# Performance work log

Measured on AMD Instinct MI355X. Metric: run time of the kernel, lower is better.

The kernel has to match this reference:

```python
import jax, jax.numpy as jnp
import numpy as np

K, N = 1024, 16384


def setup_inputs() -> dict:
    key = jax.random.key(0)
    k1, k2 = jax.random.split(key)
    # event counts per location/time step (non-negative)
    obs = jax.random.randint(k1, (K, N), 0, 5).astype(jnp.float32)
    # excitation matrix, Uniform(0, 0.01) as in the torch init
    halpha = jax.random.uniform(k2, (K, K), dtype=jnp.float32) * 0.01
    # scalar decay parameter, init 2.0
    hbeta = jnp.array([2.0], dtype=jnp.float32)
    return {"obs": obs, "halpha": halpha, "hbeta": hbeta}


def reference(obs, halpha, hbeta):
    # obs: [K, N] event counts; halpha: [K, K]; hbeta: [1]
    K_, N_ = obs.shape
    hmu = obs.mean(axis=1) / 10.0 + 0.01          # [K]
    beta = hbeta[0]
    decay = jnp.exp(-beta)

    # S_t[k] = sum_{tp < t} beta * exp(-(t - tp) * beta) * obs[k, tp]
    # Exponential kernel admits exact recursion: S_{t+1} = e^{-beta} (S_t + beta * obs_t)
    def step(S, obs_t):
        return decay * (S + beta * obs_t), S

    _, S_all = jax.lax.scan(step, jnp.zeros((K_,), obs.dtype), obs.T)  # S_all: [N, K]

    # lam1[k, t] = sum_j halpha[k, j] * S_all[t, j]   (matches mm(halpha, Nt*kernel).sum(1))
    lam1 = jnp.einsum('kj,nj->kn', halpha, S_all)      # [K, N]
    lams = jax.nn.softplus(hmu[:, None] + lam1)        # [K, N]

    loglik = (obs * jnp.log(lams) - lams).sum()
    return loglik, lams
```

## Files before the change

kernel.cpp:

```cpp
#include <hip/hip_runtime.h>

#define KDIM 1024
#define NDIM 16384
#define CHUNKS 256
#define CLEN 64
#define KTILES 16

typedef __bf16 bf16_t;
typedef bf16_t bf16x8 __attribute__((ext_vector_type(8)));
typedef bf16_t bf16x4 __attribute__((ext_vector_type(4)));
typedef float f32x4 __attribute__((ext_vector_type(4)));

__device__ __forceinline__ void gload_lds16(const bf16_t* g, bf16_t* l) {
  __builtin_amdgcn_global_load_lds(
      (const __attribute__((address_space(1))) void*)g,
      (__attribute__((address_space(3))) void*)l, 16, 0, 0);
}

__global__ __launch_bounds__(256) void k_phase1(const float* __restrict__ obs,
                                                const float* __restrict__ hbeta,
                                                float* __restrict__ carry,
                                                float* __restrict__ hmu,
                                                const float* __restrict__ A,
                                                bf16_t* __restrict__ Ab,
                                                unsigned char* __restrict__ obs8) {
  if (blockIdx.x >= 1024) {
    size_t i = ((size_t)(blockIdx.x - 1024) * 256 + threadIdx.x) * 4;
    float4 v = *reinterpret_cast<const float4*>(A + i);
    bf16x4 o;
    o[0] = (bf16_t)v.x; o[1] = (bf16_t)v.y; o[2] = (bf16_t)v.z; o[3] = (bf16_t)v.w;
    *reinterpret_cast<bf16x4*>(Ab + i) = o;
    return;
  }
  __shared__ unsigned char s8[256][68];
  __shared__ float sm[256], sa[256];
  __shared__ float wred[4];
  int tid = threadIdx.x;
  int k = blockIdx.x;
  float beta = hbeta[0];
  float decay = expf(-beta);
  const float* p = obs + (size_t)k * NDIM;
  unsigned char* po = obs8 + (size_t)k * NDIM;
  float sum = 0.f;
#pragma unroll
  for (int w = 0; w < 16; ++w) {
    float4 v = *reinterpret_cast<const float4*>(p + w * 1024 + tid * 4);
    sum += v.x + v.y + v.z + v.w;
    uchar4 u;
    u.x = (unsigned char)v.x; u.y = (unsigned char)v.y;
    u.z = (unsigned char)v.z; u.w = (unsigned char)v.w;
    *reinterpret_cast<uchar4*>(po + w * 1024 + tid * 4) = u;
    int c = w * 16 + (tid >> 4), t = 4 * (tid & 15);
    *reinterpret_cast<uchar4*>(&s8[c][t]) = u;
  }
  __syncthreads();
  float S = 0.f;
#pragma unroll 8
  for (int t = 0; t < CLEN; ++t)
    S = decay * (S + beta * (float)s8[tid][t]);
  float dL = expf(-beta * (float)CLEN);
  sm[tid] = dL; sa[tid] = S;
  __syncthreads();
#pragma unroll
  for (int s = 1; s < 256; s <<= 1) {
    float mp = 0.f, ap = 0.f;
    bool act = (tid >= s);
    if (act) { mp = sm[tid - s]; ap = sa[tid - s]; }
    __syncthreads();
    if (act) { sa[tid] += sm[tid] * ap; sm[tid] *= mp; }
    __syncthreads();
  }
  carry[(size_t)k * CHUNKS + tid] = (tid == 0) ? 0.f : sa[tid - 1];
  sum += __shfl_down(sum, 32); sum += __shfl_down(sum, 16);
  sum += __shfl_down(sum, 8);  sum += __shfl_down(sum, 4);
  sum += __shfl_down(sum, 2);  sum += __shfl_down(sum, 1);
  if ((tid & 63) == 0) wred[tid >> 6] = sum;
  __syncthreads();
  if (tid == 0)
    hmu[k] = (wred[0] + wred[1] + wred[2] + wred[3]) * (1.0f / NDIM) * 0.1f + 0.01f;
}

__global__ __launch_bounds__(64) void k_phase3(const unsigned char* __restrict__ obs8,
                                               const float* __restrict__ hbeta,
                                               const float* __restrict__ carry,
                                               bf16_t* __restrict__ S_all) {
  int c  = blockIdx.x & (CHUNKS - 1);
  int kb = blockIdx.x >> 8;
  int lane = threadIdx.x;
  float beta = hbeta[0];
  float decay = expf(-beta);
  __shared__ unsigned char s8[64][68];
  __shared__ bf16_t out_s[64][72];
  int k0 = kb * 64, t0 = c * CLEN;
  const unsigned char* base = obs8 + (size_t)k0 * NDIM + t0;
#pragma unroll 4
  for (int w = 0; w < 16; ++w) {
    int r = w * 4 + (lane >> 4), col = (lane & 15) * 4;
    *reinterpret_cast<uchar4*>(&s8[r][col]) =
        *reinterpret_cast<const uchar4*>(base + (size_t)r * NDIM + col);
  }
  __syncthreads();
  float S = carry[(size_t)(k0 + lane) * CHUNKS + c];
#pragma unroll 8
  for (int t = 0; t < CLEN; ++t) {
    out_s[t][lane] = (bf16_t)S;
    S = decay * (S + beta * (float)s8[lane][t]);
  }
  __syncthreads();
#pragma unroll 4
  for (int t = 0; t < CLEN; ++t)
    S_all[(size_t)(t0 + t) * KDIM + k0 + lane] = out_s[t][lane];
}

__global__ __launch_bounds__(512, 2) void k_gemm(const bf16_t* __restrict__ Ab,
                                                 const bf16_t* __restrict__ Bb,
                                                 const float* __restrict__ hmu,
                                                 const unsigned char* __restrict__ obs8,
                                                 float* __restrict__ out) {
  __shared__ bf16_t As[2][256 * 64];
  __shared__ bf16_t Bs[2][256 * 64];
  int tid = threadIdx.x;
  int b = blockIdx.x;
  int lb = (b & 7) * 32 + (b >> 3);
  int kb = lb & 3;
  int tb = lb >> 2;
  int lane = tid & 63, wid = tid >> 6;
  int wm = wid >> 2, wn = wid & 3;
  int r15 = lane & 15, h = lane >> 4;
  f32x4 acc[8][4] = {};

  const bf16_t* gA[4];
  const bf16_t* gB[4];
#pragma unroll
  for (int i = 0; i < 4; ++i) {
    int slot = i * 512 + tid;
    int row = slot >> 3, sp = slot & 7;
    int sl = sp ^ (row & 7);
    gA[i] = Ab + (size_t)(kb * 256 + row) * KDIM + sl * 8;
    gB[i] = Bb + (size_t)(tb * 256 + row) * KDIM + sl * 8;
  }

#define STAGE_A(buf, kkoff) do { \
  _Pragma("unroll") \
  for (int i = 0; i < 4; ++i) \
    gload_lds16(gA[i] + (kkoff), &As[buf][(i * 512 + wid * 64) * 8]); \
} while (0)
#define STAGE_B(buf, kkoff) do { \
  _Pragma("unroll") \
  for (int i = 0; i < 4; ++i) \
    gload_lds16(gB[i] + (kkoff), &Bs[buf][(i * 512 + wid * 64) * 8]); \
} while (0)

#define A_FRAG(mi, sl) (*reinterpret_cast<const bf16x8*>( \
    &As[cur][(wm * 128 + (mi) * 16 + r15) * 64 + ((((sl)) ^ ((wm * 128 + (mi) * 16 + r15) & 7)) * 8)]))
#define B_FRAG(ni, sl) (*reinterpret_cast<const bf16x8*>( \
    &Bs[cur][(wn * 64 + (ni) * 16 + r15) * 64 + ((((sl)) ^ ((wn * 64 + (ni) * 16 + r15) & 7)) * 8)]))

  STAGE_A(0, 0);
  STAGE_B(0, 0);

  int cur = 0;
  for (int kt = 0; kt < KTILES; ++kt) {
    __builtin_amdgcn_sched_barrier(0);
    __builtin_amdgcn_s_barrier();
    if (kt < KTILES - 1) {
      STAGE_A(cur ^ 1, (kt + 1) * 64);
      asm volatile("s_waitcnt vmcnt(4)" ::: "memory");
    } else {
      asm volatile("s_waitcnt vmcnt(0)" ::: "memory");
    }
    __builtin_amdgcn_s_barrier();

    bf16x8 a0[4], a1[4], bf0[4];
#pragma unroll
    for (int m = 0; m < 4; ++m) a0[m] = A_FRAG(m, h);
#pragma unroll
    for (int n = 0; n < 4; ++n) bf0[n] = B_FRAG(n, h);
    __builtin_amdgcn_s_setprio(1);
#pragma unroll
    for (int m = 0; m < 4; ++m)
#pragma unroll
      for (int n = 0; n < 4; ++n)
        acc[m][n] = __builtin_amdgcn_mfma_f32_16x16x32_bf16(a0[m], bf0[n], acc[m][n], 0, 0, 0);
    __builtin_amdgcn_s_setprio(0);
#pragma unroll
    for (int m = 0; m < 4; ++m) a1[m] = A_FRAG(4 + m, h);
    __builtin_amdgcn_s_setprio(1);
#pragma unroll
    for (int m = 0; m < 4; ++m)
#pragma unroll
      for (int n = 0; n < 4; ++n)
        acc[4 + m][n] = __builtin_amdgcn_mfma_f32_16x16x32_bf16(a1[m], bf0[n], acc[4 + m][n], 0, 0, 0);
    __builtin_amdgcn_s_setprio(0);
    if (kt < KTILES - 1) STAGE_B(cur ^ 1, (kt + 1) * 64);
#pragma unroll
    for (int m = 0; m < 4; ++m) a0[m] = A_FRAG(m, 4 + h);
#pragma unroll
    for (int n = 0; n < 4; ++n) bf0[n] = B_FRAG(n, 4 + h);
    __builtin_amdgcn_s_setprio(1);
#pragma unroll
    for (int m = 0; m < 4; ++m)
#pragma unroll
      for (int n = 0; n < 4; ++n)
        acc[m][n] = __builtin_amdgcn_mfma_f32_16x16x32_bf16(a0[m], bf0[n], acc[m][n], 0, 0, 0);
    __builtin_amdgcn_s_setprio(0);
#pragma unroll
    for (int m = 0; m < 4; ++m) a1[m] = A_FRAG(4 + m, 4 + h);
    __builtin_amdgcn_s_setprio(1);
#pragma unroll
    for (int m = 0; m < 4; ++m)
#pragma unroll
      for (int n = 0; n < 4; ++n)
        acc[4 + m][n] = __builtin_amdgcn_mfma_f32_16x16x32_bf16(a1[m], bf0[n], acc[4 + m][n], 0, 0, 0);
    __builtin_amdgcn_s_setprio(0);
    cur ^= 1;
  }
#undef STAGE_A
#undef STAGE_B
#undef A_FRAG
#undef B_FRAG

  float lsum = 0.f;
  float* lams = out + 1;
#pragma unroll
  for (int mi = 0; mi < 8; ++mi) {
    int krow0 = kb * 256 + wm * 128 + mi * 16 + h * 4;
#pragma unroll
    for (int ni = 0; ni < 4; ++ni) {
      int t = tb * 256 + wn * 64 + ni * 16 + r15;
#pragma unroll
      for (int r = 0; r < 4; ++r) {
        int krow = krow0 + r;
        float x = hmu[krow] + acc[mi][ni][r];
        float lam = fmaxf(x, 0.f) + __logf(1.f + __expf(-fabsf(x)));
        lams[(size_t)krow * NDIM + t] = lam;
        float o = (float)obs8[(size_t)krow * NDIM + t];
        lsum += o * __logf(lam) - lam;
      }
    }
  }
  lsum += __shfl_down(lsum, 32);
  lsum += __shfl_down(lsum, 16);
  lsum += __shfl_down(lsum, 8);
  lsum += __shfl_down(lsum, 4);
  lsum += __shfl_down(lsum, 2);
  lsum += __shfl_down(lsum, 1);
  __shared__ float wsum[8];
  if (lane == 0) wsum[wid] = lsum;
  __syncthreads();
  if (tid == 0) {
    float s = 0.f;
#pragma unroll
    for (int w = 0; w < 8; ++w) s += wsum[w];
    atomicAdd(out, s);
  }
}

extern "C" void kernel_launch(void* const* d_in, const int* in_sizes, int n_in,
                              void* d_out, int out_size, void* d_ws, size_t ws_size,
                              hipStream_t stream) {
  const float* obs    = (const float*)d_in[0];
  const float* halpha = (const float*)d_in[1];
  const float* hbeta  = (const float*)d_in[2];
  float* out = (float*)d_out;

  char* ws = (char*)d_ws;
  bf16_t* S_all = (bf16_t*)ws;
  float*  carry = (float*)(ws + (size_t)NDIM * KDIM * 2);
  float*  hmu   = carry + (size_t)KDIM * CHUNKS;
  bf16_t* Ab    = (bf16_t*)(hmu + KDIM);
  unsigned char* obs8 = (unsigned char*)(Ab + (size_t)KDIM * KDIM);

  hipMemsetAsync(d_out, 0, sizeof(float), stream);
  k_phase1<<<2048, 256, 0, stream>>>(obs, hbeta, carry, hmu, halpha, Ab, obs8);
  k_phase3<<<(KDIM / 64) * CHUNKS, 64, 0, stream>>>(obs8, hbeta, carry, S_all);
  k_gemm<<<4 * (NDIM / 256), 512, 0, stream>>>(Ab, S_all, hmu, obs8, out);
}
```

Measured before the change: 92.49 us.

## Restructure GEMM main loop into ping-pong schedule with interleaved partial-tile prefetch

Rewrites the bf16 MFMA main loop as a four-phase schedule. Each phase reads LDS fragments, issues part of the next tiles' global-to-LDS loads, then synchronises with barriers before a block of 16 MFMAs. Prefetch now runs up to two k-tiles ahead, split into pieces spread across phases, and B fragments are kept in registers and reused across the two M halves. The aim is to overlap global loads and LDS reads with matrix math more evenly. In exchange it adds many more workgroup barriers per k-tile, depends on hand-set vmcnt accounting, and keeps more fragments live in registers.

New measurement: 95.38 us. 1.03x slower.

```diff
diff --git a/kernel.cpp b/kernel.cpp
--- a/kernel.cpp
+++ b/kernel.cpp
@@ -140,85 +140,97 @@
     gB[i] = Bb + (size_t)(tb * 256 + row) * KDIM + sl * 8;
   }
 
-#define STAGE_A(buf, kkoff) do { \
-  _Pragma("unroll") \
-  for (int i = 0; i < 4; ++i) \
-    gload_lds16(gA[i] + (kkoff), &As[buf][(i * 512 + wid * 64) * 8]); \
-} while (0)
-#define STAGE_B(buf, kkoff) do { \
-  _Pragma("unroll") \
-  for (int i = 0; i < 4; ++i) \
-    gload_lds16(gB[i] + (kkoff), &Bs[buf][(i * 512 + wid * 64) * 8]); \
-} while (0)
-
-#define A_FRAG(mi, sl) (*reinterpret_cast<const bf16x8*>( \
-    &As[cur][(wm * 128 + (mi) * 16 + r15) * 64 + ((((sl)) ^ ((wm * 128 + (mi) * 16 + r15) & 7)) * 8)]))
-#define B_FRAG(ni, sl) (*reinterpret_cast<const bf16x8*>( \
-    &Bs[cur][(wn * 64 + (ni) * 16 + r15) * 64 + ((((sl)) ^ ((wn * 64 + (ni) * 16 + r15) & 7)) * 8)]))
-
-  STAGE_A(0, 0);
-  STAGE_B(0, 0);
-
-  int cur = 0;
-  for (int kt = 0; kt < KTILES; ++kt) {
-    __builtin_amdgcn_sched_barrier(0);
-    __builtin_amdgcn_s_barrier();
-    if (kt < KTILES - 1) {
-      STAGE_A(cur ^ 1, (kt + 1) * 64);
-      asm volatile("s_waitcnt vmcnt(4)" ::: "memory");
-    } else {
-      asm volatile("s_waitcnt vmcnt(0)" ::: "memory");
-    }
-    __builtin_amdgcn_s_barrier();
-
-    bf16x8 a0[4], a1[4], bf0[4];
-#pragma unroll
-    for (int m = 0; m < 4; ++m) a0[m] = A_FRAG(m, h);
-#pragma unroll
-    for (int n = 0; n < 4; ++n) bf0[n] = B_FRAG(n, h);
-    __builtin_amdgcn_s_setprio(1);
-#pragma unroll
-    for (int m = 0; m < 4; ++m)
-#pragma unroll
-      for (int n = 0; n < 4; ++n)
-        acc[m][n] = __builtin_amdgcn_mfma_f32_16x16x32_bf16(a0[m], bf0[n], acc[m][n], 0, 0, 0);
-    __builtin_amdgcn_s_setprio(0);
-#pragma unroll
-    for (int m = 0; m < 4; ++m) a1[m] = A_FRAG(4 + m, h);
-    __builtin_amdgcn_s_setprio(1);
-#pragma unroll
-    for (int m = 0; m < 4; ++m)
-#pragma unroll
-      for (int n = 0; n < 4; ++n)
-        acc[4 + m][n] = __builtin_amdgcn_mfma_f32_16x16x32_bf16(a1[m], bf0[n], acc[4 + m][n], 0, 0, 0);
-    __builtin_amdgcn_s_setprio(0);
-    if (kt < KTILES - 1) STAGE_B(cur ^ 1, (kt + 1) * 64);
-#pragma unroll
-    for (int m = 0; m < 4; ++m) a0[m] = A_FRAG(m, 4 + h);
-#pragma unroll
-    for (int n = 0; n < 4; ++n) bf0[n] = B_FRAG(n, 4 + h);
-    __builtin_amdgcn_s_setprio(1);
-#pragma unroll
-    for (int m = 0; m < 4; ++m)
-#pragma unroll
-      for (int n = 0; n < 4; ++n)
-        acc[m][n] = __builtin_amdgcn_mfma_f32_16x16x32_bf16(a0[m], bf0[n], acc[m][n], 0, 0, 0);
-    __builtin_amdgcn_s_setprio(0);
-#pragma unroll
-    for (int m = 0; m < 4; ++m) a1[m] = A_FRAG(4 + m, 4 + h);
-    __builtin_amdgcn_s_setprio(1);
-#pragma unroll
-    for (int m = 0; m < 4; ++m)
-#pragma unroll
-      for (int n = 0; n < 4; ++n)
-        acc[4 + m][n] = __builtin_amdgcn_mfma_f32_16x16x32_bf16(a1[m], bf0[n], acc[4 + m][n], 0, 0, 0);
-    __builtin_amdgcn_s_setprio(0);
-    cur ^= 1;
-  }
-#undef STAGE_A
-#undef STAGE_B
-#undef A_FRAG
-#undef B_FRAG
+#define SA(buf, kk, i) gload_lds16(gA[i] + (kk), &As[buf][((i) * 512 + wid * 64) * 8])
+#define SB(buf, kk, i) gload_lds16(gB[i] + (kk), &Bs[buf][((i) * 512 + wid * 64) * 8])
+#define AF(buf, mi, sl) (*reinterpret_cast<const bf16x8*>( \
+    &As[buf][(wm * 128 + (mi) * 16 + r15) * 64 + ((((sl)) ^ ((wm * 128 + (mi) * 16 + r15) & 7)) * 8)]))
+#define BF(buf, ni, sl) (*reinterpret_cast<const bf16x8*>( \
+    &Bs[buf][(wn * 64 + (ni) * 16 + r15) * 64 + ((((sl)) ^ ((wn * 64 + (ni) * 16 + r15) & 7)) * 8)]))
+#define LGKM0 do { asm volatile("s_waitcnt lgkmcnt(0)" ::: "memory"); \
+                   __builtin_amdgcn_sched_barrier(0); } while (0)
+#define SB0 __builtin_amdgcn_sched_barrier(0)
+
+  SA(0, 0, 0); SA(0, 0, 1); SA(0, 0, 2); SA(0, 0, 3);
+  SB(0, 0, 0); SB(0, 0, 1); SB(0, 0, 2); SB(0, 0, 3);
+  SB0;
+  SA(1, 64, 0); SA(1, 64, 2);
+  SB(1, 64, 0); SB(1, 64, 1); SB(1, 64, 2); SB(1, 64, 3);
+  SB0;
+  asm volatile("s_waitcnt vmcnt(6)" ::: "memory");
+  __builtin_amdgcn_s_barrier();
+
+  for (int t = 0; t < KTILES; ++t) {
+    const int cur = t & 1;
+    const int kk1 = (t + 1) * 64, kk2 = (t + 2) * 64;
+    bf16x8 a[4], bk0[4], bk1[4];
+#pragma unroll
+    for (int m = 0; m < 4; ++m) a[m] = AF(cur, m, h);
+#pragma unroll
+    for (int n = 0; n < 4; ++n) bk0[n] = BF(cur, n, h);
+    if (t + 1 < KTILES) { SA(cur ^ 1, kk1, 1); SA(cur ^ 1, kk1, 3); }
+    SB0;
+    __builtin_amdgcn_s_barrier();
+    LGKM0;
+    __builtin_amdgcn_s_setprio(1);
+#pragma unroll
+    for (int m = 0; m < 4; ++m)
+#pragma unroll
+      for (int n = 0; n < 4; ++n)
+        acc[m][n] = __builtin_amdgcn_mfma_f32_16x16x32_bf16(a[m], bk0[n], acc[m][n], 0, 0, 0);
+    __builtin_amdgcn_s_setprio(0);
+    __builtin_amdgcn_s_barrier();
+#pragma unroll
+    for (int m = 0; m < 4; ++m) a[m] = AF(cur, m, 4 + h);
+#pragma unroll
+    for (int n = 0; n < 4; ++n) bk1[n] = BF(cur, n, 4 + h);
+    SB0;
+    __builtin_amdgcn_s_barrier();
+    LGKM0;
+    __builtin_amdgcn_s_setprio(1);
+#pragma unroll
+    for (int m = 0; m < 4; ++m)
+#pragma unroll
+      for (int n = 0; n < 4; ++n)
+        acc[m][n] = __builtin_amdgcn_mfma_f32_16x16x32_bf16(a[m], bk1[n], acc[m][n], 0, 0, 0);
+    __builtin_amdgcn_s_setprio(0);
+    __builtin_amdgcn_s_barrier();
+#pragma unroll
+    for (int m = 0; m < 4; ++m) a[m] = AF(cur, 4 + m, h);
+    if (t + 2 < KTILES) { SA(cur, kk2, 0); SA(cur, kk2, 2); SB(cur, kk2, 0); SB(cur, kk2, 1); }
+    SB0;
+    __builtin_amdgcn_s_barrier();
+    LGKM0;
+    __builtin_amdgcn_s_setprio(1);
+#pragma unroll
+    for (int m = 0; m < 4; ++m)
+#pragma unroll
+      for (int n = 0; n < 4; ++n)
+        acc[4 + m][n] = __builtin_amdgcn_mfma_f32_16x16x32_bf16(a[m], bk0[n], acc[4 + m][n], 0, 0, 0);
+    __builtin_amdgcn_s_setprio(0);
+    __builtin_amdgcn_s_barrier();
+#pragma unroll
+    for (int m = 0; m < 4; ++m) a[m] = AF(cur, 4 + m, 4 + h);
+    if (t + 2 < KTILES) { SB(cur, kk2, 2); SB(cur, kk2, 3); }
+    SB0;
+    if (t <= KTILES - 3) asm volatile("s_waitcnt vmcnt(6)" ::: "memory");
+    else                 asm volatile("s_waitcnt vmcnt(0)" ::: "memory");
+    __builtin_amdgcn_s_barrier();
+    LGKM0;
+    __builtin_amdgcn_s_setprio(1);
+#pragma unroll
+    for (int m = 0; m < 4; ++m)
+#pragma unroll
+      for (int n = 0; n < 4; ++n)
+        acc[4 + m][n] = __builtin_amdgcn_mfma_f32_16x16x32_bf16(a[m], bk1[n], acc[4 + m][n], 0, 0, 0);
+    __builtin_amdgcn_s_setprio(0);
+    __builtin_amdgcn_s_barrier();
+  }
+#undef SA
+#undef SB
+#undef AF
+#undef BF
+#undef LGKM0
+#undef SB0
 
   float lsum = 0.f;
   float* lams = out + 1;
```
